# Optimization experiments

Measured on AMD Instinct MI355X. Metric: run time of the kernel, lower is better.

The kernel has to match this reference:

```python
import jax, jax.numpy as jnp
import numpy as np

EPS = 1e-8  # torch cosine_similarity norm clamp
TEMPERATURE = 1.0

B, D, H, K = 8192, 512, 1024, 11


def setup_inputs() -> dict:
    key = jax.random.key(0)
    ks = jax.random.split(key, 6)
    s1 = 1.0 / np.sqrt(D)
    s2 = 1.0 / np.sqrt(H)
    return {
        "x": jax.random.normal(ks[0], (B, D), dtype=jnp.float32),
        "Wt1": jax.random.normal(ks[1], (K, D, H), dtype=jnp.float32) * s1,
        "bt1": jnp.zeros((K, H), dtype=jnp.float32),
        "Wt2": jax.random.normal(ks[2], (K, H, D), dtype=jnp.float32) * s2,
        "bt2": jnp.zeros((K, D), dtype=jnp.float32),
        "We1": jax.random.normal(ks[3], (D, H), dtype=jnp.float32) * s1,
        "be1": jnp.zeros((H,), dtype=jnp.float32),
        "We2": jax.random.normal(ks[4], (H, H), dtype=jnp.float32) * s2,
        "be2": jnp.zeros((H,), dtype=jnp.float32),
    }


def _encode(h, We1, be1, We2, be2):
    # h: [..., D] -> [..., H]
    return jax.nn.relu(h @ We1 + be1) @ We2 + be2


def _normalize(v):
    n = jnp.sqrt(jnp.sum(v * v, axis=-1, keepdims=True))
    return v / jnp.maximum(n, EPS)


def reference(x, Wt1, bt1, Wt2, bt2, We1, be1, We2, be2):
    # K transformed views, batched: [K, B, D]
    tx = jnp.einsum("kbh,khd->kbd",
                    jnp.tanh(jnp.einsum("bd,kdh->kbh", x, Wt1) + bt1[:, None, :]),
                    Wt2) + bt2[:, None, :]
    z = _encode(x, We1, be1, We2, be2)          # [B, H]
    zk = _encode(tx, We1, be1, We2, be2)        # [K, B, H]
    zn = _normalize(z)                          # [B, H]
    zkn = _normalize(zk)                        # [K, B, H]

    inv_t = 1.0 / TEMPERATURE
    # positive sim: exp(cos(z, z_k)/T) -> [K, B]
    pos = jnp.exp(jnp.einsum("bh,kbh->kb", zn, zkn) * inv_t)
    # pairwise sims among transformed views: [K, K, B] (k <- target, l <- other)
    pair = jnp.exp(jnp.einsum("lbh,kbh->klb", zkn, zkn) * inv_t)
    diag = jnp.exp(jnp.full((K, B), inv_t, dtype=pair.dtype))  # cos(z_k,z_k)=1
    neg = pair.sum(axis=1) - diag               # sum over l != k -> [K, B]

    score = jnp.log(pos / (pos + neg))          # [K, B]
    return -score.sum(axis=0)                   # [B]
```

## Files before the change

kernel.cpp:

```cpp
#include <hip/hip_runtime.h>
#include <hip/hip_bf16.h>
#include <cstdint>
#include <cstddef>

#define NB 8192
#define ND 512
#define NH 1024
#define NK 11

typedef __bf16 bf16x8 __attribute__((ext_vector_type(8)));
typedef float f32x4 __attribute__((ext_vector_type(4)));

__global__ void cvt_f32_bf16(const float* __restrict__ in,
                             __hip_bfloat16* __restrict__ out, int n) {
  int i = blockIdx.x * blockDim.x + threadIdx.x;
  if (i < n) out[i] = __float2bfloat16(in[i]);
}

__global__ void transpose_all(const float* __restrict__ Wt1,
                              const float* __restrict__ Wt2,
                              const float* __restrict__ We1,
                              const float* __restrict__ We2,
                              __hip_bfloat16* __restrict__ Wt1t,
                              __hip_bfloat16* __restrict__ Wt2t,
                              __hip_bfloat16* __restrict__ We1t,
                              __hip_bfloat16* __restrict__ We2t) {
  __shared__ float tile[32][33];
  const int z = blockIdx.z;
  int R, C;
  const float* inb;
  __hip_bfloat16* outb;
  if (z < NK) {
    R = ND; C = NH;
    inb = Wt1 + (size_t)z * ND * NH;
    outb = Wt1t + (size_t)z * ND * NH;
  } else if (z < 2 * NK) {
    R = NH; C = ND;
    inb = Wt2 + (size_t)(z - NK) * NH * ND;
    outb = Wt2t + (size_t)(z - NK) * NH * ND;
  } else if (z == 2 * NK) {
    R = ND; C = NH;
    inb = We1; outb = We1t;
  } else {
    R = NH; C = NH;
    inb = We2; outb = We2t;
  }
  int cx = blockIdx.x * 32 + threadIdx.x;
  int ry = blockIdx.y * 32;
  if (blockIdx.x * 32 >= C || ry >= R) return;
  for (int j = threadIdx.y; j < 32; j += 8)
    tile[j][threadIdx.x] = inb[(size_t)(ry + j) * C + cx];
  __syncthreads();
  int ox = ry + threadIdx.x;
  int oy = blockIdx.x * 32;
  for (int j = threadIdx.y; j < 32; j += 8)
    outb[(size_t)(oy + j) * R + ox] = __float2bfloat16(tile[threadIdx.x][j]);
}

__device__ __forceinline__ float fast_tanh(float x) {
  float e = __expf(2.0f * x);
  return 1.0f - 2.0f / (e + 1.0f);
}

template <int EPI, int BK, int TM, int TN>
__global__ __launch_bounds__((TM / 64) * (TN / 64) * 64) void gemm_bt(
    const __hip_bfloat16* __restrict__ A, long sAz, int lda,
    const __hip_bfloat16* __restrict__ Bt, long sBz, int ldb,
    const float* __restrict__ bias, long sBiasZ,
    __hip_bfloat16* __restrict__ C, long sCz, int ldc, int Kd) {
  __shared__ __align__(16) __hip_bfloat16 As[TM * BK];
  __shared__ __align__(16) __hip_bfloat16 Bs[TN * BK];

  const int z = blockIdx.z;
  const __hip_bfloat16* Ab = A + (size_t)z * sAz;
  const __hip_bfloat16* Bb = Bt + (size_t)z * sBz;
  const float* biasb = bias + (size_t)z * sBiasZ;
  __hip_bfloat16* Cb = C + (size_t)z * sCz;

  const int bm = blockIdx.x, bn = blockIdx.y;
  const int t = threadIdx.x;
  constexpr int NWN = TN / 64;
  constexpr int T = (TM / 64) * NWN * 64;
  const int lane = t & 63, w = t >> 6;
  const int wm = w / NWN, wn = w % NWN;
  const int r = lane & 15, q = lane >> 4;

  f32x4 acc[4][4] = {};

  auto chunk_row = [&](int c) {
    return (BK == 32) ? (c >> 2) : (c >> 3);
  };
  auto chunk_gofs = [&](int c, int row) {
    return (BK == 32) ? ((((c & 3) ^ ((row >> 1) & 3)) * 8))
                      : ((((c & 7) ^ (row & 7)) * 8));
  };
  constexpr int CPTA = TM * BK / 8 / T;
  constexpr int CPTB = TN * BK / 8 / T;
  const size_t rowA = (size_t)bm * TM, rowB = (size_t)bn * TN;

  for (int k0 = 0; k0 < Kd; k0 += BK) {
#pragma unroll
    for (int m = 0; m < CPTA; ++m) {
      int c = t + m * T;
      int rw = chunk_row(c);
      __builtin_amdgcn_global_load_lds(
          (const __attribute__((address_space(1))) void*)(Ab + (rowA + rw) * lda + k0 + chunk_gofs(c, rw)),
          (__attribute__((address_space(3))) void*)(As + c * 8), 16, 0, 0);
    }
#pragma unroll
    for (int m = 0; m < CPTB; ++m) {
      int c = t + m * T;
      int rw = chunk_row(c);
      __builtin_amdgcn_global_load_lds(
          (const __attribute__((address_space(1))) void*)(Bb + (rowB + rw) * ldb + k0 + chunk_gofs(c, rw)),
          (__attribute__((address_space(3))) void*)(Bs + c * 8), 16, 0, 0);
    }
    __syncthreads();

#pragma unroll
    for (int ks = 0; ks < BK / 32; ++ks) {
      bf16x8 af[4], bfr[4];
#pragma unroll
      for (int mt = 0; mt < 4; ++mt) {
        int tr = wm * 64 + mt * 16 + r;
        int sl;
        if constexpr (BK == 32) sl = q ^ ((tr >> 1) & 3);
        else sl = (ks * 4 + q) ^ (tr & 7);
        af[mt] = *(const bf16x8*)&As[tr * BK + sl * 8];
      }
#pragma unroll
      for (int nt = 0; nt < 4; ++nt) {
        int tr = wn * 64 + nt * 16 + r;
        int sl;
        if constexpr (BK == 32) sl = q ^ ((tr >> 1) & 3);
        else sl = (ks * 4 + q) ^ (tr & 7);
        bfr[nt] = *(const bf16x8*)&Bs[tr * BK + sl * 8];
      }
#pragma unroll
      for (int mt = 0; mt < 4; ++mt)
#pragma unroll
        for (int nt = 0; nt < 4; ++nt)
          acc[mt][nt] = __builtin_amdgcn_mfma_f32_16x16x32_bf16(
              bfr[nt], af[mt], acc[mt][nt], 0, 0, 0);
    }
    __syncthreads();
  }

  const int colg0 = bn * TN + wn * 64;
  const int rowg0 = bm * TM + wm * 64;
#pragma unroll
  for (int mt = 0; mt < 4; ++mt) {
    int row = rowg0 + mt * 16 + r;
#pragma unroll
    for (int nt = 0; nt < 4; ++nt) {
      int col = colg0 + nt * 16 + q * 4;
      const f32x4 bv = *(const f32x4*)&biasb[col];
      union {
        __hip_bfloat16 h[4];
        uint2 u;
      } pk;
#pragma unroll
      for (int j = 0; j < 4; ++j) {
        float v = acc[mt][nt][j] + bv[j];
        if (EPI == 1) v = fast_tanh(v);
        if (EPI == 2) v = fmaxf(v, 0.0f);
        pk.h[j] = __float2bfloat16(v);
      }
      *(uint2*)&Cb[(size_t)row * ldc + col] = pk.u;
    }
  }
}

__global__ __launch_bounds__(256) void final_gram(
    const __hip_bfloat16* __restrict__ zc, float* __restrict__ out, int Bc) {
  __shared__ float Gs[2][2][16][16];
  const int t = threadIdx.x;
  const int w = t >> 6, lane = t & 63;
  const int bi = w >> 1;
  const int hh = w & 1;
  const int b = blockIdx.x * 2 + bi;
  const int r = lane & 15;
  const int q = lane >> 4;

  const int rs = r < 12 ? r : 11;
  const __hip_bfloat16* base =
      zc + ((size_t)b * 12 + rs) * NH + hh * (NH / 2) + q * 8;

  f32x4 acc = {};
#pragma unroll
  for (int k0 = 0; k0 < NH / 2; k0 += 32) {
    bf16x8 a = {};
    if (r < 12) a = *(const bf16x8*)(base + k0);
    acc = __builtin_amdgcn_mfma_f32_16x16x32_bf16(a, a, acc, 0, 0, 0);
  }

#pragma unroll
  for (int j = 0; j < 4; ++j) Gs[bi][hh][q * 4 + j][r] = acc[j];
  __syncthreads();

  if (hh == 0) {
    float term = 0.0f;
    if (lane >= 1 && lane < 12) {
      const float(*G0)[16] = Gs[bi][0];
      const float(*G1)[16] = Gs[bi][1];
      float nrm[12];
#pragma unroll
      for (int i = 0; i < 12; ++i)
        nrm[i] = fmaxf(sqrtf(G0[i][i] + G1[i][i]), 1e-8f);
      const int k = lane;
      float pos = __expf((G0[0][k] + G1[0][k]) / (nrm[0] * nrm[k]));
      float neg = 0.0f;
#pragma unroll
      for (int l = 1; l < 12; ++l)
        if (l != k) neg += __expf((G0[k][l] + G1[k][l]) / (nrm[k] * nrm[l]));
      term = __logf(pos / (pos + neg));
    }
#pragma unroll
    for (int m = 1; m < 16; m <<= 1) term += __shfl_xor(term, m);
    if (lane == 0) out[b] = -term;
  }
}

extern "C" void kernel_launch(void* const* d_in, const int* in_sizes, int n_in,
                              void* d_out, int out_size, void* d_ws,
                              size_t ws_size, hipStream_t stream) {
  const float* x = (const float*)d_in[0];
  const float* Wt1 = (const float*)d_in[1];
  const float* bt1 = (const float*)d_in[2];
  const float* Wt2 = (const float*)d_in[3];
  const float* bt2 = (const float*)d_in[4];
  const float* We1 = (const float*)d_in[5];
  const float* be1 = (const float*)d_in[6];
  const float* We2 = (const float*)d_in[7];
  const float* be2 = (const float*)d_in[8];
  float* out = (float*)d_out;

  char* ws = (char*)d_ws;
  size_t off = 0;
  auto alloc = [&](size_t bytes) {
    void* p = ws + off;
    off += (bytes + 255) & ~(size_t)255;
    return p;
  };

  __hip_bfloat16* Wt1t = (__hip_bfloat16*)alloc((size_t)NK * NH * ND * 2);
  __hip_bfloat16* Wt2t = (__hip_bfloat16*)alloc((size_t)NK * ND * NH * 2);
  __hip_bfloat16* We1t = (__hip_bfloat16*)alloc((size_t)NH * ND * 2);
  __hip_bfloat16* We2t = (__hip_bfloat16*)alloc((size_t)NH * NH * 2);
  const size_t wbytes = off;

  int Bc = NB;
  while (Bc > 256) {
    size_t need = wbytes + 2 * ((size_t)12 * Bc * NH * 2) + 4096;
    if (need <= ws_size) break;
    Bc >>= 1;
  }
  __hip_bfloat16* region0 = (__hip_bfloat16*)alloc((size_t)12 * Bc * NH * 2);
  __hip_bfloat16* h1 = (__hip_bfloat16*)alloc((size_t)12 * Bc * NH * 2);
  __hip_bfloat16* txc = region0;
  __hip_bfloat16* zc = region0;

  transpose_all<<<dim3(NH / 32, NH / 32, 2 * NK + 2), dim3(32, 8), 0,
                  stream>>>(Wt1, Wt2, We1, We2, Wt1t, Wt2t, We1t, We2t);

  for (int cs = 0; cs < NB; cs += Bc) {
    cvt_f32_bf16<<<(Bc * ND) / 256, 256, 0, stream>>>(
        x + (size_t)cs * ND, txc, Bc * ND);
    gemm_bt<1, 64, 256, 128><<<dim3(Bc / 256, NH / 128, NK), 512, 0,
                               stream>>>(
        txc, 0L, ND, Wt1t, (long)NH * ND, ND, bt1, (long)NH, h1,
        (long)Bc * NH, NH, ND);
    gemm_bt<3, 64, 256, 128><<<dim3(Bc / 256, ND / 128, NK), 512, 0,
                               stream>>>(
        h1, (long)Bc * NH, NH, Wt2t, (long)ND * NH, NH, bt2, (long)ND,
        txc + (size_t)Bc * ND, (long)Bc * ND, ND, NH);
    gemm_bt<2, 64, 256, 128><<<dim3(Bc / 256, NH / 128, 12), 512, 0,
                               stream>>>(
        txc, (long)Bc * ND, ND, We1t, 0L, ND, be1, 0L, h1, (long)Bc * NH,
        NH, ND);
    gemm_bt<3, 64, 256, 256><<<dim3(Bc / 256, NH / 256, 12), 1024, 0,
                               stream>>>(
        h1, (long)Bc * NH, NH, We2t, 0L, NH, be2, 0L, zc, (long)NH,
        12 * NH, NH);
    final_gram<<<Bc / 2, 256, 0, stream>>>(zc, out + cs, Bc);
  }
}
```

Baseline: 831.6 us.

## Add 256x256 ping-pong pipelined bf16 GEMM with direct global-to-LDS loads

```diff
diff --git a/kernel.cpp b/kernel.cpp
--- a/kernel.cpp
+++ b/kernel.cpp
@@ -171,6 +171,200 @@
   }
 }
 
+#define BAR8() asm volatile("s_barrier" ::: "memory")
+#define LGKM0_8()                                      \
+  do {                                                 \
+    asm volatile("s_waitcnt lgkmcnt(0)" ::: "memory"); \
+    __builtin_amdgcn_sched_barrier(0);                 \
+  } while (0)
+
+template <int EPI>
+__global__ __launch_bounds__(512, 2) void gemm8p(
+    const __hip_bfloat16* __restrict__ A, long sAz, int lda,
+    const __hip_bfloat16* __restrict__ Bt, long sBz, int ldb,
+    const float* __restrict__ bias, long sBiasZ,
+    __hip_bfloat16* __restrict__ C, long sCz, int ldc, int Kd) {
+  __shared__ __align__(16) __hip_bfloat16 As[2][2][128 * 64];
+  __shared__ __align__(16) __hip_bfloat16 Bs[2][2][128 * 64];
+
+  const int z = blockIdx.z;
+  const __hip_bfloat16* Ab = A + (size_t)z * sAz;
+  const __hip_bfloat16* Bb = Bt + (size_t)z * sBz;
+  const float* biasb = bias + (size_t)z * sBiasZ;
+  __hip_bfloat16* Cb = C + (size_t)z * sCz;
+
+  const int bm = blockIdx.x, bn = blockIdx.y;
+  const int t = threadIdx.x;
+  const int lane = t & 63, w = t >> 6;
+  const int wm = w >> 2, wn = w & 3;
+  const int r = lane & 15, q = lane >> 4;
+  const int rx = r & 7;
+  const int ao0 = (q ^ rx) * 8;
+  const int ao1 = ((4 + q) ^ rx) * 8;
+  const int brl = (wn & 1) * 64;
+
+  const size_t rowA = (size_t)bm * 256;
+  const size_t rowB = (size_t)bn * 256;
+
+  f32x4 acc[8][4] = {};
+
+  auto stage = [&](const __hip_bfloat16* gb, int ldg, size_t rbase,
+                   __hip_bfloat16* dst, int kt) {
+#pragma unroll
+    for (int i = 0; i < 2; ++i) {
+      int c = t + i * 512;
+      int rw = c >> 3;
+      int go = ((c & 7) ^ (rw & 7)) * 8;
+      __builtin_amdgcn_global_load_lds(
+          (const __attribute__((address_space(1))) void*)(
+              gb + (rbase + rw) * (size_t)ldg + kt * 64 + go),
+          (__attribute__((address_space(3))) void*)(dst + c * 8), 16, 0, 0);
+    }
+  };
+
+  auto do_tile = [&](int buf, int ktB1, int ktN, int nstage, int vmN) {
+    const __hip_bfloat16* Ap = &As[buf][wm][0];
+    const __hip_bfloat16* Bp = &Bs[buf][wn >> 1][0];
+    bf16x8 af[8][2];
+    bf16x8 bfr[2][2];
+
+#pragma unroll
+    for (int mt = 0; mt < 4; ++mt) {
+      af[mt][0] = *(const bf16x8*)&Ap[(mt * 16 + r) * 64 + ao0];
+      af[mt][1] = *(const bf16x8*)&Ap[(mt * 16 + r) * 64 + ao1];
+    }
+#pragma unroll
+    for (int nt = 0; nt < 2; ++nt) {
+      bfr[nt][0] = *(const bf16x8*)&Bp[(brl + nt * 16 + r) * 64 + ao0];
+      bfr[nt][1] = *(const bf16x8*)&Bp[(brl + nt * 16 + r) * 64 + ao1];
+    }
+    if (nstage >= 1) stage(Bb, ldb, rowB + 128, &Bs[buf ^ 1][1][0], ktB1);
+    BAR8();
+    LGKM0_8();
+    __builtin_amdgcn_s_setprio(1);
+#pragma unroll
+    for (int mt = 0; mt < 4; ++mt)
+#pragma unroll
+      for (int nt = 0; nt < 2; ++nt) {
+        acc[mt][nt] = __builtin_amdgcn_mfma_f32_16x16x32_bf16(
+            bfr[nt][0], af[mt][0], acc[mt][nt], 0, 0, 0);
+        acc[mt][nt] = __builtin_amdgcn_mfma_f32_16x16x32_bf16(
+            bfr[nt][1], af[mt][1], acc[mt][nt], 0, 0, 0);
+      }
+    __builtin_amdgcn_s_setprio(0);
+    BAR8();
+
+#pragma unroll
+    for (int mt = 4; mt < 8; ++mt) {
+      af[mt][0] = *(const bf16x8*)&Ap[(mt * 16 + r) * 64 + ao0];
+      af[mt][1] = *(const bf16x8*)&Ap[(mt * 16 + r) * 64 + ao1];
+    }
+    BAR8();
+    LGKM0_8();
+    __builtin_amdgcn_s_setprio(1);
+#pragma unroll
+    for (int mt = 4; mt < 8; ++mt)
+#pragma unroll
+      for (int nt = 0; nt < 2; ++nt) {
+        acc[mt][nt] = __builtin_amdgcn_mfma_f32_16x16x32_bf16(
+            bfr[nt][0], af[mt][0], acc[mt][nt], 0, 0, 0);
+        acc[mt][nt] = __builtin_amdgcn_mfma_f32_16x16x32_bf16(
+            bfr[nt][1], af[mt][1], acc[mt][nt], 0, 0, 0);
+      }
+    __builtin_amdgcn_s_setprio(0);
+    BAR8();
+
+#pragma unroll
+    for (int nt = 0; nt < 2; ++nt) {
+      bfr[nt][0] = *(const bf16x8*)&Bp[(brl + (nt + 2) * 16 + r) * 64 + ao0];
+      bfr[nt][1] = *(const bf16x8*)&Bp[(brl + (nt + 2) * 16 + r) * 64 + ao1];
+    }
+    if (nstage >= 4) stage(Ab, lda, rowA + 0, &As[buf][0][0], ktN);
+    BAR8();
+    LGKM0_8();
+    __builtin_amdgcn_s_setprio(1);
+#pragma unroll
+    for (int mt = 0; mt < 4; ++mt)
+#pragma unroll
+      for (int nt = 0; nt < 2; ++nt) {
+        acc[mt][nt + 2] = __builtin_amdgcn_mfma_f32_16x16x32_bf16(
+            bfr[nt][0], af[mt][0], acc[mt][nt + 2], 0, 0, 0);
+        acc[mt][nt + 2] = __builtin_amdgcn_mfma_f32_16x16x32_bf16(
+            bfr[nt][1], af[mt][1], acc[mt][nt + 2], 0, 0, 0);
+      }
+    __builtin_amdgcn_s_setprio(0);
+    BAR8();
+
+    if (nstage >= 4) {
+      stage(Ab, lda, rowA + 128, &As[buf][1][0], ktN);
+      stage(Bb, ldb, rowB + 0, &Bs[buf][0][0], ktN);
+    }
+    if (vmN == 6) {
+      asm volatile("s_waitcnt vmcnt(6)" ::: "memory");
+      __builtin_amdgcn_sched_barrier(0);
+    } else if (vmN == 0) {
+      asm volatile("s_waitcnt vmcnt(0)" ::: "memory");
+      __builtin_amdgcn_sched_barrier(0);
+    }
+    BAR8();
+    __builtin_amdgcn_s_setprio(1);
+#pragma unroll
+    for (int mt = 4; mt < 8; ++mt)
+#pragma unroll
+      for (int nt = 0; nt < 2; ++nt) {
+        acc[mt][nt + 2] = __builtin_amdgcn_mfma_f32_16x16x32_bf16(
+            bfr[nt][0], af[mt][0], acc[mt][nt + 2], 0, 0, 0);
+        acc[mt][nt + 2] = __builtin_amdgcn_mfma_f32_16x16x32_bf16(
+            bfr[nt][1], af[mt][1], acc[mt][nt + 2], 0, 0, 0);
+      }
+    __builtin_amdgcn_s_setprio(0);
+    BAR8();
+  };
+
+  stage(Ab, lda, rowA + 0, &As[0][0][0], 0);
+  stage(Ab, lda, rowA + 128, &As[0][1][0], 0);
+  stage(Bb, ldb, rowB + 0, &Bs[0][0][0], 0);
+  stage(Bb, ldb, rowB + 128, &Bs[0][1][0], 0);
+  stage(Ab, lda, rowA + 0, &As[1][0][0], 1);
+  stage(Ab, lda, rowA + 128, &As[1][1][0], 1);
+  stage(Bb, ldb, rowB + 0, &Bs[1][0][0], 1);
+  asm volatile("s_waitcnt vmcnt(6)" ::: "memory");
+  __builtin_amdgcn_sched_barrier(0);
+  BAR8();
+
+  const int NT = Kd >> 6;
+  for (int kt = 0; kt + 4 <= NT; kt += 2) {
+    do_tile(0, kt + 1, kt + 2, 4, 6);
+    do_tile(1, kt + 2, kt + 3, 4, 6);
+  }
+  do_tile(0, NT - 1, 0, 1, 0);
+  do_tile(1, 0, 0, 0, -1);
+
+  const int colg0 = bn * 256 + wn * 64;
+  const int rowg0 = bm * 256 + wm * 128;
+#pragma unroll
+  for (int mt = 0; mt < 8; ++mt) {
+    int row = rowg0 + mt * 16 + r;
+#pragma unroll
+    for (int nt = 0; nt < 4; ++nt) {
+      int col = colg0 + nt * 16 + q * 4;
+      const f32x4 bv = *(const f32x4*)&biasb[col];
+      union {
+        __hip_bfloat16 h[4];
+        uint2 u;
+      } pk;
+#pragma unroll
+      for (int j = 0; j < 4; ++j) {
+        float v = acc[mt][nt][j] + bv[j];
+        if (EPI == 1) v = fast_tanh(v);
+        if (EPI == 2) v = fmaxf(v, 0.0f);
+        pk.h[j] = __float2bfloat16(v);
+      }
+      *(uint2*)&Cb[(size_t)row * ldc + col] = pk.u;
+    }
+  }
+}
+
 __global__ __launch_bounds__(256) void final_gram(
     const __hip_bfloat16* __restrict__ zc, float* __restrict__ out, int Bc) {
   __shared__ float Gs[2][2][16][16];
@@ -266,20 +460,17 @@
   for (int cs = 0; cs < NB; cs += Bc) {
     cvt_f32_bf16<<<(Bc * ND) / 256, 256, 0, stream>>>(
         x + (size_t)cs * ND, txc, Bc * ND);
-    gemm_bt<1, 64, 256, 128><<<dim3(Bc / 256, NH / 128, NK), 512, 0,
-                               stream>>>(
+    gemm8p<1><<<dim3(Bc / 256, NH / 256, NK), 512, 0, stream>>>(
         txc, 0L, ND, Wt1t, (long)NH * ND, ND, bt1, (long)NH, h1,
         (long)Bc * NH, NH, ND);
     gemm_bt<3, 64, 256, 128><<<dim3(Bc / 256, ND / 128, NK), 512, 0,
                                stream>>>(
         h1, (long)Bc * NH, NH, Wt2t, (long)ND * NH, NH, bt2, (long)ND,
         txc + (size_t)Bc * ND, (long)Bc * ND, ND, NH);
-    gemm_bt<2, 64, 256, 128><<<dim3(Bc / 256, NH / 128, 12), 512, 0,
-                               stream>>>(
+    gemm8p<2><<<dim3(Bc / 256, NH / 256, 12), 512, 0, stream>>>(
         txc, (long)Bc * ND, ND, We1t, 0L, ND, be1, 0L, h1, (long)Bc * NH,
         NH, ND);
-    gemm_bt<3, 64, 256, 256><<<dim3(Bc / 256, NH / 256, 12), 1024, 0,
-                               stream>>>(
+    gemm8p<3><<<dim3(Bc / 256, NH / 256, 12), 512, 0, stream>>>(
         h1, (long)Bc * NH, NH, We2t, 0L, NH, be2, 0L, zc, (long)NH,
         12 * NH, NH);
     final_gram<<<Bc / 2, 256, 0, stream>>>(zc, out + cs, Bc);
```

Result: slower. 939.1 us (+12.9%).
